# Kernel tuning notes

Hardware: AMD Instinct MI355X
Metric: run time of the kernel (lower is better)

## Reference

```python
import jax, jax.numpy as jnp
import numpy as np

H = 512  # hidden_num

def _lstm_cell(x, h, c, Wih, Whh, bih, bhh):
    # PyTorch LSTMCell: gates ordered i, f, g, o
    gates = x @ Wih.T + bih + h @ Whh.T + bhh  # [B, 4H]
    i, f, g, o = jnp.split(gates, 4, axis=-1)
    i = jax.nn.sigmoid(i)
    f = jax.nn.sigmoid(f)
    g = jnp.tanh(g)
    o = jax.nn.sigmoid(o)
    c_new = f * c + i * g
    h_new = o * jnp.tanh(c_new)
    return h_new, c_new


def setup_inputs() -> dict:
    key = jax.random.key(0)
    ks = jax.random.split(key, 12)
    B, T = 256, 1024
    s1 = 1.0 / np.sqrt(H)
    u = lambda k, shape: jax.random.uniform(k, shape, jnp.float32, -s1, s1)
    return {
        "input": jax.random.normal(ks[0], (B, T), dtype=jnp.float32),
        "pred_len": 64,
        "Wih1": u(ks[1], (4 * H, 1)),
        "Whh1": u(ks[2], (4 * H, H)),
        "bih1": u(ks[3], (4 * H,)),
        "bhh1": u(ks[4], (4 * H,)),
        "Wih2": u(ks[5], (4 * H, H)),
        "Whh2": u(ks[6], (4 * H, H)),
        "bih2": u(ks[7], (4 * H,)),
        "bhh2": u(ks[8], (4 * H,)),
        "Wlin": u(ks[9], (1, H)),
        "blin": u(ks[10], (1,)),
    }


def reference(input, pred_len, Wih1, Whh1, bih1, bhh1, Wih2, Whh2, bih2, bhh2, Wlin, blin):
    B = input.shape[0]
    z = jnp.zeros((B, H), dtype=input.dtype)
    xs = input.T[:, :, None]  # [T, B, 1]

    def step(carry, x_t):
        h1, c1, h2, c2 = carry
        h1, c1 = _lstm_cell(x_t, h1, c1, Wih1, Whh1, bih1, bhh1)
        h2, c2 = _lstm_cell(h1, h2, c2, Wih2, Whh2, bih2, bhh2)
        return (h1, c1, h2, c2), None

    (h1, c1, h2, c2), _ = jax.lax.scan(step, (z, z, z, z), xs)
    out = h2 @ Wlin.T + blin  # [B, 1]
    first = out[-1, :]        # [1]

    def ar_step(carry, _):
        h1, c1, h2, c2, o = carry
        h1, c1 = _lstm_cell(o, h1, c1, Wih1, Whh1, bih1, bhh1)
        h2, c2 = _lstm_cell(h1, h2, c2, Wih2, Whh2, bih2, bhh2)
        o = h2 @ Wlin.T + blin
        return (h1, c1, h2, c2, o), o[-1, :]

    if pred_len - 1 > 0:
        _, ys = jax.lax.scan(ar_step, (h1, c1, h2, c2, out), None, length=pred_len - 1)
        return jnp.concatenate([first, ys.reshape(-1)])  # [pred_len]
    return first
```

## Files before the change

### kernel.cpp

```cpp
#include <hip/hip_runtime.h>
#include <math.h>


#define G     64
#define NT    512
#define HD    512
#define TT    1024
#define PRED  64
#define LINEF 64
#define SLOTF (G*LINEF)
#define STR   264
#define AS    __HIP_MEMORY_SCOPE_AGENT

typedef unsigned long long u64;

#define LOG2E  1.44269504088896340736f

#define KEEP4(v) asm volatile("" : "+v"(v.x), "+v"(v.y), "+v"(v.z), "+v"(v.w))

__device__ __forceinline__ float sigf(float x){
  return __builtin_amdgcn_rcpf(1.0f + __builtin_amdgcn_exp2f(-LOG2E * x));
}
__device__ __forceinline__ float tanhf_fast(float x){
  float e = __builtin_amdgcn_exp2f(2.0f * LOG2E * x);
  return 1.0f - 2.0f * __builtin_amdgcn_rcpf(e + 1.0f);
}
__device__ __forceinline__ float dot4(float4 a, float4 b){
  return a.x*b.x + a.y*b.y + a.z*b.z + a.w*b.w;
}

__global__ __launch_bounds__(NT, 1) void lstm2_kernel(
    const float* __restrict__ input,
    const float* __restrict__ Wih1, const float* __restrict__ Whh1,
    const float* __restrict__ bih1, const float* __restrict__ bhh1,
    const float* __restrict__ Wih2, const float* __restrict__ Whh2,
    const float* __restrict__ bih2, const float* __restrict__ bhh2,
    const float* __restrict__ Wlin, const float* __restrict__ blin,
    float* __restrict__ out, float* __restrict__ ws)
{
  __shared__ __align__(16) float hvec[4*STR];
  __shared__ __align__(16) float xrow[TT];
  __shared__ float pre[64];

  float* comm = ws;

  const int t  = threadIdx.x;
  const int wg = blockIdx.x;
  const int rg = t >> 6;
  const int sg = t & 63;

  ((float2*)xrow)[t] = ((const float2*)(input + 255*TT))[t];

  float4 w1[4][2], w2[4][4];
  #pragma unroll
  for (int k=0;k<4;k++){
    const int r = rg*4 + k;
    const int R = (r>>3)*HD + wg*8 + (r&7);
    const float* pa = Whh1 + R*HD + sg*8;
    w1[k][0] = *(const float4*)(pa);
    w1[k][1] = *(const float4*)(pa+4);
    const float* pb = Wih2 + R*HD + sg*8;
    const float* pc = Whh2 + R*HD + sg*8;
    w2[k][0] = *(const float4*)(pb);
    w2[k][1] = *(const float4*)(pb+4);
    w2[k][2] = *(const float4*)(pc);
    w2[k][3] = *(const float4*)(pc+4);
  }
  #pragma unroll
  for (int k=0;k<4;k++){
    KEEP4(w1[k][0]); KEEP4(w1[k][1]);
    KEEP4(w2[k][0]); KEEP4(w2[k][1]); KEEP4(w2[k][2]); KEEP4(w2[k][3]);
  }

  float bias[4]={0,0,0,0}, wx[4]={0,0,0,0};
  float cst  = 0.f;
  float hcur = 0.f;
  if (t < 8){
    #pragma unroll
    for (int q=0;q<4;q++){
      int R = q*HD + wg*8 + t;
      bias[q] = bih1[R] + bhh1[R];
      wx[q]   = Wih1[R];
    }
  } else if (t < 16){
    #pragma unroll
    for (int q=0;q<4;q++){
      int R = q*HD + wg*8 + (t-8);
      bias[q] = bih2[R] + bhh2[R];
    }
  }
  float4 wl0={0,0,0,0}, wl1={0,0,0,0};
  if (t < 64){
    wl0 = *(const float4*)(Wlin + t*8);
    wl1 = *(const float4*)(Wlin + t*8 + 4);
  }
  const float blin0 = blin[0];

  auto poll_stage = [&](unsigned g){
    const int w = t >> 3, j = t & 7;
    const u64* dq = (const u64*)(comm + (g & 1u)*SLOTF + w*LINEF) + 2*j;
    u64 q0, q1;
    do {
      q0 = __hip_atomic_load(dq,     __ATOMIC_RELAXED, AS);
      q1 = __hip_atomic_load(dq + 1, __ATOMIC_RELAXED, AS);
    } while ((unsigned)(q0 >> 32) != g || (unsigned)(q1 >> 32) != g);
    const int c  = j >> 1;
    const int wd = c*STR + 4*w + 2*(j & 1);
    float2 fv;
    fv.x = __builtin_bit_cast(float, (unsigned)q0);
    fv.y = __builtin_bit_cast(float, (unsigned)q1);
    *(float2*)(hvec + wd) = fv;
    __syncthreads();
  };

  auto dots_reduce = [&](){
    const float4 c0 = ((const float4*)(hvec + 0*STR))[sg];
    const float4 c1 = ((const float4*)(hvec + 1*STR))[sg];
    const float4 c2 = ((const float4*)(hvec + 2*STR))[sg];
    const float4 c3 = ((const float4*)(hvec + 3*STR))[sg];
    float v[8];
    #pragma unroll
    for (int k=0;k<4;k++){
      v[k]   = dot4(w1[k][0],c0) + dot4(w1[k][1],c1);
      v[4+k] = dot4(w2[k][0],c0) + dot4(w2[k][1],c1)
             + dot4(w2[k][2],c2) + dot4(w2[k][3],c3);
    }
    const int b0 = sg & 1, b1 = (sg>>1)&1, b2 = (sg>>2)&1;
    float k4[4];
    #pragma unroll
    for (int k=0;k<4;k++){
      float x = b0 ? v[k] : v[k+4];
      float y = __shfl_xor(x, 1, 64);
      k4[k] = (b0 ? v[k+4] : v[k]) + y;
    }
    float k2[2];
    #pragma unroll
    for (int k=0;k<2;k++){
      float x = b1 ? k4[k] : k4[k+2];
      float y = __shfl_xor(x, 2, 64);
      k2[k] = (b1 ? k4[k+2] : k4[k]) + y;
    }
    float k1;
    {
      float x = b2 ? k2[0] : k2[1];
      float y = __shfl_xor(x, 4, 64);
      k1 = (b2 ? k2[1] : k2[0]) + y;
    }
    k1 += __shfl_xor(k1, 8, 64);
    k1 += __shfl_xor(k1, 16, 64);
    k1 += __shfl_xor(k1, 32, 64);
    if (sg < 8){
      const int j = b0*4 + b1*2 + b2;
      if (j < 4) pre[rg*4 + j]        = k1;
      else       pre[32 + rg*4 + j-4] = k1;
    }
  };

  auto tail = [&](unsigned g, bool d1, bool d2, float xv){
    if (rg == 0){
      const float rsum = pre[t];
      const int u  = t & 7;
      const int s0 = (t < 8) ? t : (32 + u);
      float pi = __shfl(rsum, s0,      64);
      float pf = __shfl(rsum, s0 + 8,  64);
      float pg = __shfl(rsum, s0 + 16, 64);
      float po = __shfl(rsum, s0 + 24, 64);
      const bool act = (t < 8) ? d1 : ((t < 16) ? d2 : false);
      if (act){
        if (t < 8){
          pi += xv*wx[0] + bias[0];
          pf += xv*wx[1] + bias[1];
          pg += xv*wx[2] + bias[2];
          po += xv*wx[3] + bias[3];
        } else {
          pi += bias[0]; pf += bias[1]; pg += bias[2]; po += bias[3];
        }
        cst  = sigf(pf)*cst + sigf(pi)*tanhf_fast(pg);
        hcur = sigf(po)*tanhf_fast(cst);
      }
      if (t < 16){
        u64 pr = ((u64)(g + 1u) << 32) | (u64)__builtin_bit_cast(unsigned, hcur);
        u64* nb = (u64*)(comm + ((g+1u) & 1u)*SLOTF + wg*LINEF);
        __hip_atomic_store(nb + t, pr, __ATOMIC_RELAXED, AS);
      }
    }
  };

  auto computeO = [&](int oi, float& xv){
    if (rg == 0){
      float s = dot4(wl0, ((const float4*)(hvec + 2*STR))[t])
              + dot4(wl1, ((const float4*)(hvec + 3*STR))[t]);
      #pragma unroll
      for (int m=1;m<64;m<<=1) s += __shfl_xor(s, m, 64);
      xv = s + blin0;
      if (wg == 0 && t == 0) out[oi] = xv;
    }
  };

  __syncthreads();

  unsigned g = 0;

  for (int tk=0; tk<TT; ++tk, ++g){
    poll_stage(g);
    dots_reduce();
    __syncthreads();
    tail(g, true, tk >= 1, xrow[tk]);
  }

  poll_stage(g);
  dots_reduce();
  __syncthreads();
  tail(g, false, true, 0.f);
  ++g;

  for (int s=TT; s<TT+PRED-1; ++s){
    poll_stage(g);
    float xv = 0.f;
    computeO(s - TT, xv);
    dots_reduce();
    __syncthreads();
    tail(g, true, false, xv);
    ++g;

    poll_stage(g);
    dots_reduce();
    __syncthreads();
    tail(g, false, true, 0.f);
    ++g;
  }

  poll_stage(g);
  float xv;
  computeO(PRED - 1, xv);
}

extern "C" void kernel_launch(void* const* d_in, const int* in_sizes, int n_in,
                              void* d_out, int out_size, void* d_ws, size_t ws_size,
                              hipStream_t stream) {
  const float* input = (const float*)d_in[0];
  const float* Wih1 = (const float*)d_in[2];
  const float* Whh1 = (const float*)d_in[3];
  const float* bih1 = (const float*)d_in[4];
  const float* bhh1 = (const float*)d_in[5];
  const float* Wih2 = (const float*)d_in[6];
  const float* Whh2 = (const float*)d_in[7];
  const float* bih2 = (const float*)d_in[8];
  const float* bhh2 = (const float*)d_in[9];
  const float* Wlin = (const float*)d_in[10];
  const float* blin = (const float*)d_in[11];

  hipMemsetAsync(d_ws, 0, 2 * SLOTF * sizeof(float), stream);

  lstm2_kernel<<<dim3(G), dim3(NT), 0, stream>>>(
      input, Wih1, Whh1, bih1, bhh1, Wih2, Whh2, bih2, bhh2, Wlin, blin,
      (float*)d_out, (float*)d_ws);
}
```

Measured before the change: 2.065 ms.

## Remap rows per wavefront and double-buffer hvec to drop a block barrier

```diff
diff --git a/kernel.cpp b/kernel.cpp
--- a/kernel.cpp
+++ b/kernel.cpp
@@ -10,6 +10,7 @@
 #define LINEF 64
 #define SLOTF (G*LINEF)
 #define STR   264
+#define HVS   (4*STR)
 #define AS    __HIP_MEMORY_SCOPE_AGENT
 
 typedef unsigned long long u64;
@@ -38,9 +39,8 @@
     const float* __restrict__ Wlin, const float* __restrict__ blin,
     float* __restrict__ out, float* __restrict__ ws)
 {
-  __shared__ __align__(16) float hvec[4*STR];
+  __shared__ __align__(16) float hvec[2*HVS];
   __shared__ __align__(16) float xrow[TT];
-  __shared__ float pre[64];
 
   float* comm = ws;
 
@@ -54,8 +54,7 @@
   float4 w1[4][2], w2[4][4];
   #pragma unroll
   for (int k=0;k<4;k++){
-    const int r = rg*4 + k;
-    const int R = (r>>3)*HD + wg*8 + (r&7);
+    const int R = k*HD + wg*8 + rg;
     const float* pa = Whh1 + R*HD + sg*8;
     w1[k][0] = *(const float4*)(pa);
     w1[k][1] = *(const float4*)(pa+4);
@@ -75,25 +74,16 @@
   float bias[4]={0,0,0,0}, wx[4]={0,0,0,0};
   float cst  = 0.f;
   float hcur = 0.f;
-  if (t < 8){
+  if (sg < 2){
     #pragma unroll
     for (int q=0;q<4;q++){
-      int R = q*HD + wg*8 + t;
-      bias[q] = bih1[R] + bhh1[R];
-      wx[q]   = Wih1[R];
-    }
-  } else if (t < 16){
-    #pragma unroll
-    for (int q=0;q<4;q++){
-      int R = q*HD + wg*8 + (t-8);
-      bias[q] = bih2[R] + bhh2[R];
-    }
-  }
-  float4 wl0={0,0,0,0}, wl1={0,0,0,0};
-  if (t < 64){
-    wl0 = *(const float4*)(Wlin + t*8);
-    wl1 = *(const float4*)(Wlin + t*8 + 4);
-  }
+      const int R = q*HD + wg*8 + rg;
+      if (sg == 0){ bias[q] = bih1[R] + bhh1[R]; wx[q] = Wih1[R]; }
+      else        { bias[q] = bih2[R] + bhh2[R]; }
+    }
+  }
+  const float4 wl0 = *(const float4*)(Wlin + sg*8);
+  const float4 wl1 = *(const float4*)(Wlin + sg*8 + 4);
   const float blin0 = blin[0];
 
   auto poll_stage = [&](unsigned g){
@@ -105,7 +95,7 @@
       q1 = __hip_atomic_load(dq + 1, __ATOMIC_RELAXED, AS);
     } while ((unsigned)(q0 >> 32) != g || (unsigned)(q1 >> 32) != g);
     const int c  = j >> 1;
-    const int wd = c*STR + 4*w + 2*(j & 1);
+    const int wd = (int)(g & 1u)*HVS + c*STR + 4*w + 2*(j & 1);
     float2 fv;
     fv.x = __builtin_bit_cast(float, (unsigned)q0);
     fv.y = __builtin_bit_cast(float, (unsigned)q1);
@@ -113,11 +103,12 @@
     __syncthreads();
   };
 
-  auto dots_reduce = [&](){
-    const float4 c0 = ((const float4*)(hvec + 0*STR))[sg];
-    const float4 c1 = ((const float4*)(hvec + 1*STR))[sg];
-    const float4 c2 = ((const float4*)(hvec + 2*STR))[sg];
-    const float4 c3 = ((const float4*)(hvec + 3*STR))[sg];
+  auto dots_reduce = [&](unsigned g)->float{
+    const float* hb = hvec + (g & 1u)*HVS;
+    const float4 c0 = ((const float4*)(hb + 0*STR))[sg];
+    const float4 c1 = ((const float4*)(hb + 1*STR))[sg];
+    const float4 c2 = ((const float4*)(hb + 2*STR))[sg];
+    const float4 c3 = ((const float4*)(hb + 3*STR))[sg];
     float v[8];
     #pragma unroll
     for (int k=0;k<4;k++){
@@ -149,25 +140,19 @@
     k1 += __shfl_xor(k1, 8, 64);
     k1 += __shfl_xor(k1, 16, 64);
     k1 += __shfl_xor(k1, 32, 64);
-    if (sg < 8){
-      const int j = b0*4 + b1*2 + b2;
-      if (j < 4) pre[rg*4 + j]        = k1;
-      else       pre[32 + rg*4 + j-4] = k1;
-    }
-  };
-
-  auto tail = [&](unsigned g, bool d1, bool d2, float xv){
-    if (rg == 0){
-      const float rsum = pre[t];
-      const int u  = t & 7;
-      const int s0 = (t < 8) ? t : (32 + u);
-      float pi = __shfl(rsum, s0,      64);
-      float pf = __shfl(rsum, s0 + 8,  64);
-      float pg = __shfl(rsum, s0 + 16, 64);
-      float po = __shfl(rsum, s0 + 24, 64);
-      const bool act = (t < 8) ? d1 : ((t < 16) ? d2 : false);
+    return k1;
+  };
+
+  auto tick_tail = [&](unsigned g, bool d1, bool d2, float xv, float k1){
+    const int r = sg & 1;
+    float pi = __shfl(k1, r,     64);
+    float pf = __shfl(k1, r + 4, 64);
+    float pg = __shfl(k1, r + 2, 64);
+    float po = __shfl(k1, r + 6, 64);
+    if (sg < 2){
+      const bool act = (r == 0) ? d1 : d2;
       if (act){
-        if (t < 8){
+        if (r == 0){
           pi += xv*wx[0] + bias[0];
           pf += xv*wx[1] + bias[1];
           pg += xv*wx[2] + bias[2];
@@ -178,61 +163,54 @@
         cst  = sigf(pf)*cst + sigf(pi)*tanhf_fast(pg);
         hcur = sigf(po)*tanhf_fast(cst);
       }
-      if (t < 16){
-        u64 pr = ((u64)(g + 1u) << 32) | (u64)__builtin_bit_cast(unsigned, hcur);
-        u64* nb = (u64*)(comm + ((g+1u) & 1u)*SLOTF + wg*LINEF);
-        __hip_atomic_store(nb + t, pr, __ATOMIC_RELAXED, AS);
-      }
-    }
-  };
-
-  auto computeO = [&](int oi, float& xv){
-    if (rg == 0){
-      float s = dot4(wl0, ((const float4*)(hvec + 2*STR))[t])
-              + dot4(wl1, ((const float4*)(hvec + 3*STR))[t]);
-      #pragma unroll
-      for (int m=1;m<64;m<<=1) s += __shfl_xor(s, m, 64);
-      xv = s + blin0;
-      if (wg == 0 && t == 0) out[oi] = xv;
-    }
-  };
-
-  __syncthreads();
+      u64 pr = ((u64)(g + 1u) << 32) | (u64)__builtin_bit_cast(unsigned, hcur);
+      u64* nb = (u64*)(comm + ((g+1u) & 1u)*SLOTF + wg*LINEF);
+      __hip_atomic_store(nb + (r ? 8 + rg : rg), pr, __ATOMIC_RELAXED, AS);
+    }
+  };
+
+  auto computeO = [&](unsigned g)->float{
+    const float* hb = hvec + (g & 1u)*HVS;
+    float s = dot4(wl0, ((const float4*)(hb + 2*STR))[sg])
+            + dot4(wl1, ((const float4*)(hb + 3*STR))[sg]);
+    #pragma unroll
+    for (int m=1;m<64;m<<=1) s += __shfl_xor(s, m, 64);
+    return s + blin0;
+  };
 
   unsigned g = 0;
 
   for (int tk=0; tk<TT; ++tk, ++g){
     poll_stage(g);
-    dots_reduce();
-    __syncthreads();
-    tail(g, true, tk >= 1, xrow[tk]);
+    const float xv = xrow[tk];
+    const float k1 = dots_reduce(g);
+    tick_tail(g, true, tk >= 1, xv, k1);
   }
 
   poll_stage(g);
-  dots_reduce();
-  __syncthreads();
-  tail(g, false, true, 0.f);
+  {
+    const float k1 = dots_reduce(g);
+    tick_tail(g, false, true, 0.f, k1);
+  }
   ++g;
 
   for (int s=TT; s<TT+PRED-1; ++s){
     poll_stage(g);
-    float xv = 0.f;
-    computeO(s - TT, xv);
-    dots_reduce();
-    __syncthreads();
-    tail(g, true, false, xv);
+    const float xv = computeO(g);
+    if (wg == 0 && t == 0) out[s - TT] = xv;
+    float k1 = dots_reduce(g);
+    tick_tail(g, true, false, xv, k1);
     ++g;
 
     poll_stage(g);
-    dots_reduce();
-    __syncthreads();
-    tail(g, false, true, 0.f);
+    k1 = dots_reduce(g);
+    tick_tail(g, false, true, 0.f, k1);
     ++g;
   }
 
   poll_stage(g);
-  float xv;
-  computeO(PRED - 1, xv);
+  const float xv = computeO(g);
+  if (wg == 0 && t == 0) out[PRED - 1] = xv;
 }
 
 extern "C" void kernel_launch(void* const* d_in, const int* in_sizes, int n_in,
```

Result: slower. 3.686 ms (+78.5%).

## Halve workgroup count to 32 with 1024 threads each, 16 hidden units per group

Applied to the files above, without the earlier changes.

```diff
diff --git a/kernel.cpp b/kernel.cpp
--- a/kernel.cpp
+++ b/kernel.cpp
@@ -2,13 +2,13 @@
 #include <math.h>
 
 
-#define G     64
-#define NT    512
+#define G     32
+#define NT    1024
 #define HD    512
 #define TT    1024
 #define PRED  64
-#define LINEF 64
-#define SLOTF (G*LINEF)
+#define LINEU 32
+#define SLOTU (G*LINEU)
 #define STR   264
 #define AS    __HIP_MEMORY_SCOPE_AGENT
 
@@ -40,22 +40,22 @@
 {
   __shared__ __align__(16) float hvec[4*STR];
   __shared__ __align__(16) float xrow[TT];
-  __shared__ float pre[64];
-
-  float* comm = ws;
+  __shared__ float pre[128];
+
+  u64* commu = (u64*)ws;
 
   const int t  = threadIdx.x;
   const int wg = blockIdx.x;
   const int rg = t >> 6;
   const int sg = t & 63;
 
-  ((float2*)xrow)[t] = ((const float2*)(input + 255*TT))[t];
+  xrow[t] = input[255*TT + t];
 
   float4 w1[4][2], w2[4][4];
   #pragma unroll
   for (int k=0;k<4;k++){
     const int r = rg*4 + k;
-    const int R = (r>>3)*HD + wg*8 + (r&7);
+    const int R = (r>>4)*HD + wg*16 + (r&15);
     const float* pa = Whh1 + R*HD + sg*8;
     w1[k][0] = *(const float4*)(pa);
     w1[k][1] = *(const float4*)(pa+4);
@@ -75,17 +75,17 @@
   float bias[4]={0,0,0,0}, wx[4]={0,0,0,0};
   float cst  = 0.f;
   float hcur = 0.f;
-  if (t < 8){
+  if (t < 16){
     #pragma unroll
     for (int q=0;q<4;q++){
-      int R = q*HD + wg*8 + t;
+      int R = q*HD + wg*16 + t;
       bias[q] = bih1[R] + bhh1[R];
       wx[q]   = Wih1[R];
     }
-  } else if (t < 16){
+  } else if (t < 32){
     #pragma unroll
     for (int q=0;q<4;q++){
-      int R = q*HD + wg*8 + (t-8);
+      int R = q*HD + wg*16 + (t-16);
       bias[q] = bih2[R] + bhh2[R];
     }
   }
@@ -97,19 +97,15 @@
   const float blin0 = blin[0];
 
   auto poll_stage = [&](unsigned g){
-    const int w = t >> 3, j = t & 7;
-    const u64* dq = (const u64*)(comm + (g & 1u)*SLOTF + w*LINEF) + 2*j;
-    u64 q0, q1;
-    do {
-      q0 = __hip_atomic_load(dq,     __ATOMIC_RELAXED, AS);
-      q1 = __hip_atomic_load(dq + 1, __ATOMIC_RELAXED, AS);
-    } while ((unsigned)(q0 >> 32) != g || (unsigned)(q1 >> 32) != g);
-    const int c  = j >> 1;
-    const int wd = c*STR + 4*w + 2*(j & 1);
-    float2 fv;
-    fv.x = __builtin_bit_cast(float, (unsigned)q0);
-    fv.y = __builtin_bit_cast(float, (unsigned)q1);
-    *(float2*)(hvec + wd) = fv;
+    const int w = t >> 5, i = t & 31;
+    const u64* dq = commu + (g & 1u)*SLOTU + w*LINEU + i;
+    u64 q0;
+    do { q0 = __hip_atomic_load(dq, __ATOMIC_RELAXED, AS); }
+    while ((unsigned)(q0 >> 32) != g);
+    const int U  = w*16 + (i & 15);
+    const int c  = ((i < 16) ? 0 : 2) + ((U >> 2) & 1);
+    const int wd = c*STR + 4*(U >> 3) + (U & 3);
+    hvec[wd] = __builtin_bit_cast(float, (unsigned)q0);
     __syncthreads();
   };
 
@@ -152,22 +148,30 @@
     if (sg < 8){
       const int j = b0*4 + b1*2 + b2;
       if (j < 4) pre[rg*4 + j]        = k1;
-      else       pre[32 + rg*4 + j-4] = k1;
+      else       pre[64 + rg*4 + j-4] = k1;
     }
   };
 
   auto tail = [&](unsigned g, bool d1, bool d2, float xv){
     if (rg == 0){
-      const float rsum = pre[t];
-      const int u  = t & 7;
-      const int s0 = (t < 8) ? t : (32 + u);
-      float pi = __shfl(rsum, s0,      64);
-      float pf = __shfl(rsum, s0 + 8,  64);
-      float pg = __shfl(rsum, s0 + 16, 64);
-      float po = __shfl(rsum, s0 + 24, 64);
-      const bool act = (t < 8) ? d1 : ((t < 16) ? d2 : false);
+      const float rsumA = pre[t];
+      const float rsumB = pre[64 + t];
+      const int u = t & 15;
+      float pi, pf, pg, po;
+      {
+        float a0 = __shfl(rsumA, u,      64), b0_ = __shfl(rsumB, u,      64);
+        float a1 = __shfl(rsumA, u + 16, 64), b1_ = __shfl(rsumB, u + 16, 64);
+        float a2 = __shfl(rsumA, u + 32, 64), b2_ = __shfl(rsumB, u + 32, 64);
+        float a3 = __shfl(rsumA, u + 48, 64), b3_ = __shfl(rsumB, u + 48, 64);
+        const bool l1 = (t < 16);
+        pi = l1 ? a0 : b0_;
+        pf = l1 ? a1 : b1_;
+        pg = l1 ? a2 : b2_;
+        po = l1 ? a3 : b3_;
+      }
+      const bool act = (t < 16) ? d1 : ((t < 32) ? d2 : false);
       if (act){
-        if (t < 8){
+        if (t < 16){
           pi += xv*wx[0] + bias[0];
           pf += xv*wx[1] + bias[1];
           pg += xv*wx[2] + bias[2];
@@ -178,10 +182,10 @@
         cst  = sigf(pf)*cst + sigf(pi)*tanhf_fast(pg);
         hcur = sigf(po)*tanhf_fast(cst);
       }
-      if (t < 16){
+      if (t < 32){
         u64 pr = ((u64)(g + 1u) << 32) | (u64)__builtin_bit_cast(unsigned, hcur);
-        u64* nb = (u64*)(comm + ((g+1u) & 1u)*SLOTF + wg*LINEF);
-        __hip_atomic_store(nb + t, pr, __ATOMIC_RELAXED, AS);
+        u64* nb = commu + ((g+1u) & 1u)*SLOTU + wg*LINEU + t;
+        __hip_atomic_store(nb, pr, __ATOMIC_RELAXED, AS);
       }
     }
   };
@@ -250,7 +254,7 @@
   const float* Wlin = (const float*)d_in[10];
   const float* blin = (const float*)d_in[11];
 
-  hipMemsetAsync(d_ws, 0, 2 * SLOTF * sizeof(float), stream);
+  hipMemsetAsync(d_ws, 0, (size_t)2 * SLOTU * sizeof(u64), stream);
 
   lstm2_kernel<<<dim3(G), dim3(NT), 0, stream>>>(
       input, Wih1, Whh1, bih1, bhh1, Wih2, Whh2, bih2, bhh2, Wlin, blin,
```

Result: slower. 5.466 ms (+164.7%).
